# Kernel optimization log

Measured on AMD Instinct MI355X. Metric: run time of the kernel, lower is better.

Reference implementation:

```python
import jax, jax.numpy as jnp
import numpy as np

HEADS = 8
GROUPS = 8            # offset_groups (defaults to heads)
DIM = 256
DIM_HEAD = 64
INNER = HEADS * DIM_HEAD          # 512
OFF_DIMS = INNER // GROUPS        # 64
DS = 4                            # downsample_factor
OFF_SCALE = float(DS)             # offset_scale defaults to downsample_factor
KS = 6                            # offset_kernel_size
SCALE = DIM_HEAD ** -0.5


def grouped_conv1x1(x, w, groups):
    # x: (B, Cin, N), w: (Cout, Cin//groups, 1) -> (B, Cout, N)
    B, Cin, N = x.shape
    Cout = w.shape[0]
    xg = x.reshape(B, groups, Cin // groups, N)
    wg = w[:, :, 0].reshape(groups, Cout // groups, Cin // groups)
    return jnp.einsum('bgin,goi->bgon', xg, wg).reshape(B, Cout, N)


def group(t, groups):
    # 'b (g d) n -> (b g) d n'
    B, C, N = t.shape
    return t.reshape(B, groups, C // groups, N).reshape(B * groups, C // groups, N)


def bilinear_sample_1d(feats, grid):
    # F.grid_sample 1d equivalent: bilinear, padding_mode='zeros', align_corners=False
    # feats: (B, C, N); grid: (B, M) in [-1, 1] -> (B, C, M)
    B, C, N = feats.shape
    pos = ((grid + 1.0) * N - 1.0) * 0.5     # unnormalized coordinate
    i0f = jnp.floor(pos)
    w1 = (pos - i0f)[:, None, :]
    i0 = i0f.astype(jnp.int32)

    def gather(idx):
        valid = ((idx >= 0) & (idx < N))[:, None, :].astype(feats.dtype)
        g = jnp.take_along_axis(feats, jnp.clip(idx, 0, N - 1)[:, None, :], axis=2)
        return g * valid

    return gather(i0) * (1.0 - w1) + gather(i0 + 1) * w1


def setup_inputs() -> dict:
    key = jax.random.key(0)
    ks = jax.random.split(key, 10)
    B, N = 4, 4096
    s = lambda k, shape, fan: jax.random.normal(k, shape, jnp.float32) * (fan ** -0.5)
    return {
        'x': jax.random.normal(ks[0], (B, N, DIM), jnp.float32),
        'prev_x': jax.random.normal(ks[1], (B, N, DIM), jnp.float32),
        'wq': s(ks[2], (INNER, 2 * DIM // GROUPS, 1), 2 * DIM // GROUPS),
        'wk': s(ks[3], (INNER, DIM // GROUPS, 1), DIM // GROUPS),
        'wv': s(ks[4], (INNER, DIM // GROUPS, 1), DIM // GROUPS),
        'wo': s(ks[5], (DIM, INNER, 1), INNER),
        'bo': jnp.zeros((DIM,), jnp.float32),
        'w_off1': s(ks[6], (OFF_DIMS, 1, KS), KS),      # depthwise conv, groups=OFF_DIMS
        'b_off1': jnp.zeros((OFF_DIMS,), jnp.float32),
        'w_off2': s(ks[7], (1, OFF_DIMS, 1), OFF_DIMS),  # 1x1 conv, no bias
    }


def reference(x, prev_x, wq, wk, wv, wo, bo, w_off1, b_off1, w_off2):
    B, N, _ = x.shape
    xt = jnp.swapaxes(x, 1, 2)        # (B, D, N)
    pt = jnp.swapaxes(prev_x, 1, 2)   # (B, D, N)
    cat = jnp.concatenate([pt, xt], axis=1)       # (B, 2D, N)

    q = grouped_conv1x1(cat, wq, GROUPS)          # (B, INNER, N)
    gq = group(q, GROUPS)                         # (B*G, OFF_DIMS, N)

    # to_offsets: depthwise conv (stride DS) -> GELU -> 1x1 -> tanh -> *scale
    pad = (KS - DS) // 2
    h = jax.lax.conv_general_dilated(
        gq, w_off1, (DS,), [(pad, pad)],
        dimension_numbers=('NCH', 'OIH', 'NCH'),
        feature_group_count=OFF_DIMS)
    h = jax.nn.gelu(h + b_off1[None, :, None], approximate=False)  # (B*G, OFF_DIMS, M)
    offsets = jnp.einsum('bcn,oc->bon', h, w_off2[:, :, 0])[:, 0]  # (B*G, M)
    offsets = jnp.tanh(offsets) * OFF_SCALE

    M = offsets.shape[-1]                          # downsampled kv length
    vgrid = jnp.arange(M, dtype=offsets.dtype) + offsets
    vgrid_scaled = 2.0 * vgrid / max(M - 1, 1) - 1.0

    kv = bilinear_sample_1d(group(pt, GROUPS), vgrid_scaled)       # (B*G, D/G, M)
    kv = kv.reshape(B, GROUPS, DIM // GROUPS, M).reshape(B, DIM, M)

    k = grouped_conv1x1(kv, wk, GROUPS)            # (B, INNER, M)
    v = grouped_conv1x1(kv, wv, GROUPS)            # (B, INNER, M)

    # 'b (h d) n -> b h n d'
    qh = (q * SCALE).reshape(B, HEADS, DIM_HEAD, N).transpose(0, 1, 3, 2)
    kh = k.reshape(B, HEADS, DIM_HEAD, M).transpose(0, 1, 3, 2)
    vh = v.reshape(B, HEADS, DIM_HEAD, M).transpose(0, 1, 3, 2)

    attn = jax.nn.softmax(jnp.einsum('bhid,bhjd->bhij', qh, kh), axis=-1)
    out = jnp.einsum('bhij,bhjd->bhid', attn, vh)  # (B, H, N, Dh)

    out = out.transpose(0, 1, 3, 2).reshape(B, INNER, N)
    out = jnp.einsum('bcn,oc->bon', out, wo[:, :, 0]) + bo[None, :, None]
    return jnp.swapaxes(out, 1, 2)                 # (B, N, D)
```

## Files before the change

kernel.cpp:

```cpp
#include <hip/hip_runtime.h>
#include <hip/hip_bf16.h>

#define NN 4096
#define DIMC 256
#define NH 8
#define MM 1024
#define SCALE 0.18033688011112042f

typedef __hip_bfloat16 bf16;
typedef __bf16 bf16x8 __attribute__((ext_vector_type(8)));
typedef __bf16 bf16x4 __attribute__((ext_vector_type(4)));
typedef float f32x4 __attribute__((ext_vector_type(4)));
typedef unsigned u32x4 __attribute__((ext_vector_type(4)));
#define MFMA16(a, b, c) __builtin_amdgcn_mfma_f32_16x16x32_bf16(a, b, c, 0, 0, 0)

#define CVTPK(d, a, b) asm("v_cvt_pk_bf16_f32 %0, %1, %2" : "=v"(d) : "v"(a), "v"(b))
#define SWAP32(a, b) asm("v_permlane32_swap_b32 %0, %1" : "+v"(a), "+v"(b))
#define SWAP16(a, b) asm("v_permlane16_swap_b32 %0, %1" : "+v"(a), "+v"(b))

typedef __bf16 lds_row72[72];

__device__ __forceinline__ float bf2f(bf16 v) { return __bfloat162float(v); }
__device__ __forceinline__ float ldin(const void* p, size_t i, int f) {
    return f ? __bfloat162float(((const bf16*)p)[i]) : ((const float*)p)[i];
}
__device__ __forceinline__ bf16x8 ld8bf(const void* p, size_t i, int f) {
    if (f) return *(const bf16x8*)((const __bf16*)p + i);
    const float* s = (const float*)p + i;
    float4 a = *(const float4*)s, b = *(const float4*)(s + 4);
    bf16x8 r = {(__bf16)a.x, (__bf16)a.y, (__bf16)a.z, (__bf16)a.w,
                (__bf16)b.x, (__bf16)b.y, (__bf16)b.z, (__bf16)b.w};
    return r;
}

__global__ __launch_bounds__(256) void detect_kernel(const unsigned short* __restrict__ xu,
                                                     int* __restrict__ flag) {
    __shared__ int smax;
    int t = threadIdx.x;
    if (t == 0) smax = 0;
    __syncthreads();
    int mymax = 0;
    for (int i = t; i < 4096; i += 256) {
        int e = (xu[i] >> 7) & 0xFF;
        mymax = max(mymax, e);
    }
    atomicMax(&smax, mymax);
    __syncthreads();
    if (t == 0) *flag = (smax >= 0x90) ? 0 : 1;
}

__global__ __launch_bounds__(256) void off_kernel(
    const void* __restrict__ xp, const void* __restrict__ pxp,
    const void* __restrict__ wqp, const void* __restrict__ w1p,
    const void* __restrict__ b1p, const void* __restrict__ w2p,
    float* __restrict__ offs, const int* __restrict__ flagp) {
    __shared__ __align__(16) float wq_lds[64][68];
    __shared__ __align__(16) float cat_lds[66][68];
    __shared__ float q_lds[66][68];
    int f = *flagp;
    int t = threadIdx.x;
    int bg = blockIdx.x >> 6;
    int m0 = (blockIdx.x & 63) << 4;
    int b = bg >> 3, g = bg & 7;
    const void* src = (g < 4) ? pxp : xp;
    int base = (g & 3) << 6;
    for (int idx = t; idx < 4096; idx += 256)
        wq_lds[idx >> 6][idx & 63] = ldin(wqp, g * 4096 + idx, f);
    for (int idx = t; idx < 66 * 64; idx += 256) {
        int r = idx >> 6, c = idx & 63;
        int n = 4 * m0 - 1 + r;
        cat_lds[r][c] = (n >= 0 && n < NN)
            ? ldin(src, ((size_t)b * NN + n) * DIMC + base + c, f) : 0.0f;
    }
    __syncthreads();
    {
        int tc = t & 15, tr = t >> 4;
        float acc[4][4];
#pragma unroll
        for (int a = 0; a < 4; ++a)
#pragma unroll
            for (int bb = 0; bb < 4; ++bb) acc[a][bb] = 0.f;
#pragma unroll
        for (int i4 = 0; i4 < 16; ++i4) {
            float4 cv[4], wv[4];
#pragma unroll
            for (int a = 0; a < 4; ++a)
                cv[a] = *(const float4*)&cat_lds[tr + 16 * a][i4 * 4];
#pragma unroll
            for (int bb = 0; bb < 4; ++bb)
                wv[bb] = *(const float4*)&wq_lds[tc + 16 * bb][i4 * 4];
#pragma unroll
            for (int a = 0; a < 4; ++a)
#pragma unroll
                for (int bb = 0; bb < 4; ++bb) {
                    acc[a][bb] += cv[a].x * wv[bb].x;
                    acc[a][bb] += cv[a].y * wv[bb].y;
                    acc[a][bb] += cv[a].z * wv[bb].z;
                    acc[a][bb] += cv[a].w * wv[bb].w;
                }
        }
#pragma unroll
        for (int a = 0; a < 4; ++a)
#pragma unroll
            for (int bb = 0; bb < 4; ++bb)
                q_lds[tr + 16 * a][tc + 16 * bb] = acc[a][bb];
        if (t < 128) {
            int r = 64 + (t >> 6), c = t & 63;
            float a2 = 0.f;
#pragma unroll
            for (int i4 = 0; i4 < 16; ++i4) {
                float4 cv = *(const float4*)&cat_lds[r][i4 * 4];
                float4 wv = *(const float4*)&wq_lds[c][i4 * 4];
                a2 += cv.x * wv.x;
                a2 += cv.y * wv.y;
                a2 += cv.z * wv.z;
                a2 += cv.w * wv.w;
            }
            q_lds[r][c] = a2;
        }
    }
    __syncthreads();
    int w = t >> 6, lane = t & 63;
    float w1v[6];
#pragma unroll
    for (int tap = 0; tap < 6; ++tap) w1v[tap] = ldin(w1p, lane * 6 + tap, f);
    float b1v = ldin(b1p, lane, f);
    float w2v = ldin(w2p, lane, f);
    for (int jj = 0; jj < 4; ++jj) {
        int dm = w * 4 + jj;
        int r0 = 4 * dm;
        float acc = b1v;
#pragma unroll
        for (int tap = 0; tap < 6; ++tap) acc += q_lds[r0 + tap][lane] * w1v[tap];
        float gl = 0.5f * acc * (1.0f + erff(acc * 0.70710678118654752f));
        float s = gl * w2v;
#pragma unroll
        for (int o = 32; o; o >>= 1) s += __shfl_xor(s, o);
        if (lane == 0) offs[bg * MM + m0 + dm] = tanhf(s) * 4.0f;
    }
}

__global__ __launch_bounds__(256) void kvproj_kernel(
    const void* __restrict__ pxp, const void* __restrict__ wkp,
    const void* __restrict__ wvp, const float* __restrict__ offs,
    __bf16* __restrict__ khi_g, __bf16* __restrict__ klo_g,
    __bf16* __restrict__ vt_g, const int* __restrict__ flagp) {
    __shared__ float wk_lds[64][33];
    __shared__ float wv_lds[64][33];
    __shared__ float kv_lds[64][33];
    __shared__ __align__(16) __bf16 vt_lds[64][72];
    __shared__ float offl[64];
    int f = *flagp;
    int t = threadIdx.x;
    int bh = blockIdx.x >> 4;
    int m0 = (blockIdx.x & 15) << 6;
    int b = bh >> 3, h = bh & 7;
    if (t < 64) offl[t] = offs[bh * MM + m0 + t];
    for (int kk = t; kk < 2048; kk += 256) {
        wk_lds[kk >> 5][kk & 31] = ldin(wkp, h * 2048 + kk, f);
        wv_lds[kk >> 5][kk & 31] = ldin(wvp, h * 2048 + kk, f);
    }
    __syncthreads();
    for (int idx = t; idx < 2048; idx += 256) {
        int ml = idx >> 5, i = idx & 31;
        int m = m0 + ml;
        float off = offl[ml];
        float vgrid = (float)m + off;
        float gridn = 2.0f * vgrid / 1023.0f - 1.0f;
        float pos = ((gridn + 1.0f) * 4096.0f - 1.0f) * 0.5f;
        float i0f = floorf(pos);
        float w1 = pos - i0f;
        int i0 = (int)i0f;
        size_t basep = (size_t)b * NN * DIMC + h * 32 + i;
        float v0 = (i0 >= 0 && i0 < NN) ? ldin(pxp, basep + (size_t)i0 * DIMC, f) : 0.0f;
        int i1 = i0 + 1;
        float v1 = (i1 >= 0 && i1 < NN) ? ldin(pxp, basep + (size_t)i1 * DIMC, f) : 0.0f;
        kv_lds[ml][i] = v0 * (1.0f - w1) + v1 * w1;
    }
    __syncthreads();
    int d = t & 63, msub = t >> 6;
    for (int mc = 0; mc < 16; ++mc) {
        int ml = mc * 4 + msub;
        float ak = 0.f, av = 0.f;
#pragma unroll
        for (int i = 0; i < 32; ++i) {
            float x = kv_lds[ml][i];
            ak += x * wk_lds[d][i];
            av += x * wv_lds[d][i];
        }
        int m = m0 + ml;
        __bf16 kh = (__bf16)ak;
        khi_g[(size_t)(bh * MM + m) * 64 + d] = kh;
        klo_g[(size_t)(bh * MM + m) * 64 + d] = (__bf16)(ak - (float)kh);
        vt_lds[d][ml] = (__bf16)av;
    }
    __syncthreads();
    for (int idx = t; idx < 512; idx += 256) {
        int r = idx >> 3, c8 = (idx & 7) * 8;
        *(bf16x8*)&vt_g[((size_t)bh * 64 + r) * MM + m0 + c8] =
            *(const bf16x8*)&vt_lds[r][c8];
    }
}

__global__ __launch_bounds__(256, 4) void attn_kernel(
    const void* __restrict__ xp, const void* __restrict__ pxp,
    const void* __restrict__ wqp, const __bf16* __restrict__ khi_g,
    const __bf16* __restrict__ klo_g, const __bf16* __restrict__ vt_g,
    __bf16* __restrict__ ofb, const int* __restrict__ flagp) {
    __shared__ __align__(16) char smem[36864];
    int f = *flagp;
    int bh = blockIdx.x >> 5;
    int n0 = (blockIdx.x & 31) << 7;
    int b = bh >> 3, h = bh & 7;
    int t = threadIdx.x;
    int w = t >> 6, lane = t & 63;
    int quad = lane >> 4, l15 = lane & 15;

    lds_row72* x_lds  = (lds_row72*)smem;
    lds_row72* wq_lds = (lds_row72*)(smem + 18432);
    const void* src = (h < 4) ? pxp : xp;
    int cbase = (h & 3) << 6;
#pragma unroll
    for (int j = 0; j < 4; ++j) {
        int idx = t + j * 256;
        int r = idx >> 3, c8 = (idx & 7) * 8;
        *(bf16x8*)&x_lds[r][c8] =
            ld8bf(src, ((size_t)b * NN + n0 + r) * DIMC + cbase + c8, f);
    }
#pragma unroll
    for (int j = 0; j < 2; ++j) {
        int idx = t + j * 256;
        int r = idx >> 3, c8 = (idx & 7) * 8;
        *(bf16x8*)&wq_lds[r][c8] = ld8bf(wqp, h * 4096 + r * 64 + c8, f);
    }
    __syncthreads();
    bf16x8 axf[2][2], bwf[4][2];
#pragma unroll
    for (int ms = 0; ms < 2; ++ms)
#pragma unroll
        for (int ks = 0; ks < 2; ++ks)
            axf[ms][ks] = *(const bf16x8*)&x_lds[w * 32 + ms * 16 + l15][quad * 8 + ks * 32];
#pragma unroll
    for (int ns = 0; ns < 4; ++ns)
#pragma unroll
        for (int ks = 0; ks < 2; ++ks)
            bwf[ns][ks] = *(const bf16x8*)&wq_lds[ns * 16 + l15][quad * 8 + ks * 32];
    __syncthreads();
    lds_row72* qhi = (lds_row72*)smem;
    lds_row72* qlo = (lds_row72*)(smem + 18432);
#pragma unroll
    for (int ms = 0; ms < 2; ++ms)
#pragma unroll
        for (int ns = 0; ns < 4; ++ns) {
            f32x4 acc = {0.f, 0.f, 0.f, 0.f};
            acc = MFMA16(axf[ms][0], bwf[ns][0], acc);
            acc = MFMA16(axf[ms][1], bwf[ns][1], acc);
            int col = ns * 16 + l15;
#pragma unroll
            for (int reg = 0; reg < 4; ++reg) {
                int row = w * 32 + ms * 16 + quad * 4 + reg;
                float v = acc[reg] * SCALE;
                __bf16 hi = (__bf16)v;
                qhi[row][col] = hi;
                qlo[row][col] = (__bf16)(v - (float)hi);
            }
        }
    __syncthreads();
    bf16x8 qh[2][2], ql[2][2];
#pragma unroll
    for (int ms = 0; ms < 2; ++ms)
#pragma unroll
        for (int ks = 0; ks < 2; ++ks) {
            qh[ms][ks] = *(const bf16x8*)&qhi[w * 32 + ms * 16 + l15][quad * 8 + ks * 32];
            ql[ms][ks] = *(const bf16x8*)&qlo[w * 32 + ms * 16 + l15][quad * 8 + ks * 32];
        }

    lds_row72* khi = (lds_row72*)smem;
    lds_row72* klo = (lds_row72*)(smem + 9216);
    lds_row72* vt  = (lds_row72*)(smem + 18432);

    float l_run[2] = {0.f, 0.f};
    f32x4 oc[2][4];
#pragma unroll
    for (int ms = 0; ms < 2; ++ms)
#pragma unroll
        for (int nd = 0; nd < 4; ++nd) oc[ms][nd] = (f32x4){0.f, 0.f, 0.f, 0.f};

    const __bf16* khb = khi_g + (size_t)bh * MM * 64;
    const __bf16* klb = klo_g + (size_t)bh * MM * 64;
    const __bf16* vtb = vt_g + (size_t)bh * 64 * MM;

    int pr0 = t >> 3, pc0 = (t & 7) * 8;
    int pr1 = (t + 256) >> 3, pc1 = pc0;
    bf16x8 pk[2], pl[2], pv[2];
    {
        pk[0] = *(const bf16x8*)&khb[(size_t)pr0 * 64 + pc0];
        pk[1] = *(const bf16x8*)&khb[(size_t)pr1 * 64 + pc1];
        pl[0] = *(const bf16x8*)&klb[(size_t)pr0 * 64 + pc0];
        pl[1] = *(const bf16x8*)&klb[(size_t)pr1 * 64 + pc1];
        pv[0] = *(const bf16x8*)&vtb[(size_t)pr0 * MM + pc0];
        pv[1] = *(const bf16x8*)&vtb[(size_t)pr1 * MM + pc1];
    }

    for (int mt = 0; mt < 16; ++mt) {
        __syncthreads();
        *(bf16x8*)&khi[pr0][pc0] = pk[0];
        *(bf16x8*)&khi[pr1][pc1] = pk[1];
        *(bf16x8*)&klo[pr0][pc0] = pl[0];
        *(bf16x8*)&klo[pr1][pc1] = pl[1];
        *(bf16x8*)&vt[pr0][pc0]  = pv[0];
        *(bf16x8*)&vt[pr1][pc1]  = pv[1];
        __syncthreads();
        if (mt < 15) {
            int m1 = (mt + 1) * 64;
            pk[0] = *(const bf16x8*)&khb[(size_t)(m1 + pr0) * 64 + pc0];
            pk[1] = *(const bf16x8*)&khb[(size_t)(m1 + pr1) * 64 + pc1];
            pl[0] = *(const bf16x8*)&klb[(size_t)(m1 + pr0) * 64 + pc0];
            pl[1] = *(const bf16x8*)&klb[(size_t)(m1 + pr1) * 64 + pc1];
            pv[0] = *(const bf16x8*)&vtb[(size_t)pr0 * MM + m1 + pc0];
            pv[1] = *(const bf16x8*)&vtb[(size_t)pr1 * MM + m1 + pc1];
        }
        f32x4 s[2][4];
#pragma unroll
        for (int ms = 0; ms < 2; ++ms)
#pragma unroll
            for (int nk = 0; nk < 4; ++nk) s[ms][nk] = (f32x4){0.f, 0.f, 0.f, 0.f};
#pragma unroll
        for (int nk = 0; nk < 4; ++nk)
#pragma unroll
            for (int ks = 0; ks < 2; ++ks) {
                bf16x8 kh = *(const bf16x8*)&khi[nk * 16 + l15][quad * 8 + ks * 32];
                bf16x8 kl = *(const bf16x8*)&klo[nk * 16 + l15][quad * 8 + ks * 32];
#pragma unroll
                for (int ms = 0; ms < 2; ++ms) {
                    s[ms][nk] = MFMA16(kh, qh[ms][ks], s[ms][nk]);
                    s[ms][nk] = MFMA16(kl, qh[ms][ks], s[ms][nk]);
                    s[ms][nk] = MFMA16(kh, ql[ms][ks], s[ms][nk]);
                }
            }
        bf16x8 pf[2][2];
#pragma unroll
        for (int ms = 0; ms < 2; ++ms) {
            float ps = 0.f;
#pragma unroll
            for (int nk = 0; nk < 4; ++nk)
#pragma unroll
                for (int reg = 0; reg < 4; ++reg) {
                    float v = exp2f(s[ms][nk][reg] - 16.f);
                    s[ms][nk][reg] = v;
                    ps += v;
                }
            ps += __shfl_xor(ps, 16);
            ps += __shfl_xor(ps, 32);
            l_run[ms] += ps;
#pragma unroll
            for (int ks = 0; ks < 2; ++ks) {
                unsigned a0, a1, b0, b1;
                CVTPK(a0, s[ms][2 * ks][0], s[ms][2 * ks][1]);
                CVTPK(a1, s[ms][2 * ks][2], s[ms][2 * ks][3]);
                CVTPK(b0, s[ms][2 * ks + 1][0], s[ms][2 * ks + 1][1]);
                CVTPK(b1, s[ms][2 * ks + 1][2], s[ms][2 * ks + 1][3]);
                SWAP32(a0, b0);
                SWAP32(a1, b1);
                SWAP16(a0, b0);
                SWAP16(a1, b1);
                u32x4 wrd = {a0, a1, b0, b1};
                pf[ms][ks] = *(const bf16x8*)&wrd;
            }
        }
#pragma unroll
        for (int nd = 0; nd < 4; ++nd)
#pragma unroll
            for (int ks = 0; ks < 2; ++ks) {
                bf16x8 vf_ = *(const bf16x8*)&vt[nd * 16 + l15][quad * 8 + ks * 32];
#pragma unroll
                for (int ms = 0; ms < 2; ++ms)
                    oc[ms][nd] = MFMA16(pf[ms][ks], vf_, oc[ms][nd]);
            }
    }
#pragma unroll
    for (int ms = 0; ms < 2; ++ms)
#pragma unroll
        for (int reg = 0; reg < 4; ++reg) {
            float lsum = __shfl(l_run[ms], quad * 4 + reg);
            float rl = 1.0f / lsum;
            int n = n0 + w * 32 + ms * 16 + quad * 4 + reg;
#pragma unroll
            for (int nd = 0; nd < 4; ++nd)
                ofb[((size_t)b * NN + n) * 512 + h * 64 + nd * 16 + l15] =
                    (__bf16)(oc[ms][nd][reg] * rl);
        }
}

__global__ __launch_bounds__(256) void o_proj_kernel(
    const __bf16* __restrict__ ofb, const void* __restrict__ wop,
    const void* __restrict__ bop, void* __restrict__ out,
    const int* __restrict__ flagp) {
    __shared__ __align__(16) char smem[27648];
    lds_row72* ahi = (lds_row72*)smem;
    lds_row72* bwo = (lds_row72*)(smem + 18432);
    int f = *flagp;
    int t = threadIdx.x;
    int row0 = (blockIdx.x >> 2) * 128;
    int o0 = (blockIdx.x & 3) * 64;
    int w = t >> 6, lane = t & 63;
    int quad = lane >> 4, l15 = lane & 15;

    f32x4 oc[2][4];
#pragma unroll
    for (int ms = 0; ms < 2; ++ms)
#pragma unroll
        for (int nd = 0; nd < 4; ++nd) oc[ms][nd] = (f32x4){0.f, 0.f, 0.f, 0.f};

    for (int k0 = 0; k0 < 512; k0 += 64) {
        if (k0) __syncthreads();
#pragma unroll
        for (int j = 0; j < 4; ++j) {
            int idx = t + j * 256;
            int r = idx >> 3, c8 = (idx & 7) * 8;
            *(bf16x8*)&ahi[r][c8] =
                *(const bf16x8*)&ofb[(size_t)(row0 + r) * 512 + k0 + c8];
        }
#pragma unroll
        for (int j = 0; j < 2; ++j) {
            int idx = t + j * 256;
            int o = idx >> 3, c8 = (idx & 7) * 8;
            *(bf16x8*)&bwo[o][c8] = ld8bf(wop, (size_t)(o0 + o) * 512 + k0 + c8, f);
        }
        __syncthreads();
        bf16x8 af[2][2], bf_[4][2];
#pragma unroll
        for (int ms = 0; ms < 2; ++ms)
#pragma unroll
            for (int ks = 0; ks < 2; ++ks)
                af[ms][ks] = *(const bf16x8*)&ahi[w * 32 + ms * 16 + l15][quad * 8 + ks * 32];
#pragma unroll
        for (int nd = 0; nd < 4; ++nd)
#pragma unroll
            for (int ks = 0; ks < 2; ++ks)
                bf_[nd][ks] = *(const bf16x8*)&bwo[nd * 16 + l15][quad * 8 + ks * 32];
#pragma unroll
        for (int ms = 0; ms < 2; ++ms)
#pragma unroll
            for (int nd = 0; nd < 4; ++nd)
#pragma unroll
                for (int ks = 0; ks < 2; ++ks)
                    oc[ms][nd] = MFMA16(af[ms][ks], bf_[nd][ks], oc[ms][nd]);
    }
    float bias[4];
#pragma unroll
    for (int nd = 0; nd < 4; ++nd) bias[nd] = ldin(bop, o0 + nd * 16 + l15, f);
#pragma unroll
    for (int ms = 0; ms < 2; ++ms)
#pragma unroll
        for (int reg = 0; reg < 4; ++reg) {
            int grow = row0 + w * 32 + ms * 16 + quad * 4 + reg;
#pragma unroll
            for (int nd = 0; nd < 4; ++nd) {
                float v = oc[ms][nd][reg] + bias[nd];
                int o = o0 + nd * 16 + l15;
                if (f) ((bf16*)out)[(size_t)grow * 256 + o] = __float2bfloat16(v);
                else   ((float*)out)[(size_t)grow * 256 + o] = v;
            }
        }
}

extern "C" void kernel_launch(void* const* d_in, const int* in_sizes, int n_in,
                              void* d_out, int out_size, void* d_ws, size_t ws_size,
                              hipStream_t stream) {
    char* W = (char*)d_ws;
    int* flag = (int*)W;
    __bf16* khi_g = (__bf16*)(W + 256);
    __bf16* klo_g = khi_g + 2097152;
    __bf16* vt_g  = klo_g + 2097152;
    __bf16* ofb   = vt_g + 2097152;
    float* offs = (float*)(ofb + 8388608);

    hipLaunchKernelGGL(detect_kernel, dim3(1), dim3(256), 0, stream,
                       (const unsigned short*)d_in[0], flag);
    hipLaunchKernelGGL(off_kernel, dim3(2048), dim3(256), 0, stream,
                       d_in[0], d_in[1], d_in[2], d_in[7], d_in[8], d_in[9],
                       offs, flag);
    hipLaunchKernelGGL(kvproj_kernel, dim3(512), dim3(256), 0, stream,
                       d_in[1], d_in[3], d_in[4], offs, khi_g, klo_g, vt_g, flag);
    hipLaunchKernelGGL(attn_kernel, dim3(1024), dim3(256), 0, stream,
                       d_in[0], d_in[1], d_in[2], khi_g, klo_g, vt_g, ofb, flag);
    hipLaunchKernelGGL(o_proj_kernel, dim3(512), dim3(256), 0, stream,
                       ofb, d_in[5], d_in[6], d_out, flag);
}
```

Measured before the change: 265.7 us.

## Halve attention query tile and KV tile to raise occupancy; cache kv weights in registers

The attention kernel now handles 64 query rows per block instead of 128 and streams K/V in 32-row tiles instead of 64. This halves shared memory and register use and lets launch bounds request 8 blocks per CU, with twice as many blocks launched. The aim is to improve latency hiding for the attention stage. In exchange, each K/V tile is loaded from global memory by twice as many blocks and the loop runs twice as many iterations with barriers. Separately, the kv projection keeps its weight columns in registers instead of rereading them from LDS, and s_setprio hints are placed around the MFMA sections.

Result: slower. 387.2 us (+45.7%).

```diff
diff --git a/kernel.cpp b/kernel.cpp
--- a/kernel.cpp
+++ b/kernel.cpp
@@ -19,6 +19,7 @@
 #define SWAP16(a, b) asm("v_permlane16_swap_b32 %0, %1" : "+v"(a), "+v"(b))
 
 typedef __bf16 lds_row72[72];
+typedef __bf16 lds_row40[40];
 
 __device__ __forceinline__ float bf2f(bf16 v) { return __bfloat162float(v); }
 __device__ __forceinline__ float ldin(const void* p, size_t i, int f) {
@@ -179,14 +180,20 @@
     }
     __syncthreads();
     int d = t & 63, msub = t >> 6;
+    float wkr[32], wvr[32];
+#pragma unroll
+    for (int i = 0; i < 32; ++i) {
+        wkr[i] = wk_lds[d][i];
+        wvr[i] = wv_lds[d][i];
+    }
     for (int mc = 0; mc < 16; ++mc) {
         int ml = mc * 4 + msub;
         float ak = 0.f, av = 0.f;
 #pragma unroll
         for (int i = 0; i < 32; ++i) {
             float x = kv_lds[ml][i];
-            ak += x * wk_lds[d][i];
-            av += x * wv_lds[d][i];
+            ak += x * wkr[i];
+            av += x * wvr[i];
         }
         int m = m0 + ml;
         __bf16 kh = (__bf16)ak;
@@ -202,44 +209,37 @@
     }
 }
 
-__global__ __launch_bounds__(256, 4) void attn_kernel(
+__global__ __launch_bounds__(256, 8) void attn_kernel(
     const void* __restrict__ xp, const void* __restrict__ pxp,
     const void* __restrict__ wqp, const __bf16* __restrict__ khi_g,
     const __bf16* __restrict__ klo_g, const __bf16* __restrict__ vt_g,
     __bf16* __restrict__ ofb, const int* __restrict__ flagp) {
-    __shared__ __align__(16) char smem[36864];
+    __shared__ __align__(16) char smem[18432];
     int f = *flagp;
-    int bh = blockIdx.x >> 5;
-    int n0 = (blockIdx.x & 31) << 7;
+    int bh = blockIdx.x >> 6;
+    int n0 = (blockIdx.x & 63) << 6;
     int b = bh >> 3, h = bh & 7;
     int t = threadIdx.x;
     int w = t >> 6, lane = t & 63;
     int quad = lane >> 4, l15 = lane & 15;
 
     lds_row72* x_lds  = (lds_row72*)smem;
-    lds_row72* wq_lds = (lds_row72*)(smem + 18432);
+    lds_row72* wq_lds = (lds_row72*)(smem + 9216);
     const void* src = (h < 4) ? pxp : xp;
     int cbase = (h & 3) << 6;
 #pragma unroll
-    for (int j = 0; j < 4; ++j) {
+    for (int j = 0; j < 2; ++j) {
         int idx = t + j * 256;
         int r = idx >> 3, c8 = (idx & 7) * 8;
         *(bf16x8*)&x_lds[r][c8] =
             ld8bf(src, ((size_t)b * NN + n0 + r) * DIMC + cbase + c8, f);
-    }
-#pragma unroll
-    for (int j = 0; j < 2; ++j) {
-        int idx = t + j * 256;
-        int r = idx >> 3, c8 = (idx & 7) * 8;
         *(bf16x8*)&wq_lds[r][c8] = ld8bf(wqp, h * 4096 + r * 64 + c8, f);
     }
     __syncthreads();
-    bf16x8 axf[2][2], bwf[4][2];
-#pragma unroll
-    for (int ms = 0; ms < 2; ++ms)
-#pragma unroll
-        for (int ks = 0; ks < 2; ++ks)
-            axf[ms][ks] = *(const bf16x8*)&x_lds[w * 32 + ms * 16 + l15][quad * 8 + ks * 32];
+    bf16x8 axf[2], bwf[4][2];
+#pragma unroll
+    for (int ks = 0; ks < 2; ++ks)
+        axf[ks] = *(const bf16x8*)&x_lds[w * 16 + l15][quad * 8 + ks * 32];
 #pragma unroll
     for (int ns = 0; ns < 4; ++ns)
 #pragma unroll
@@ -247,149 +247,118 @@
             bwf[ns][ks] = *(const bf16x8*)&wq_lds[ns * 16 + l15][quad * 8 + ks * 32];
     __syncthreads();
     lds_row72* qhi = (lds_row72*)smem;
-    lds_row72* qlo = (lds_row72*)(smem + 18432);
-#pragma unroll
-    for (int ms = 0; ms < 2; ++ms)
-#pragma unroll
-        for (int ns = 0; ns < 4; ++ns) {
-            f32x4 acc = {0.f, 0.f, 0.f, 0.f};
-            acc = MFMA16(axf[ms][0], bwf[ns][0], acc);
-            acc = MFMA16(axf[ms][1], bwf[ns][1], acc);
-            int col = ns * 16 + l15;
-#pragma unroll
-            for (int reg = 0; reg < 4; ++reg) {
-                int row = w * 32 + ms * 16 + quad * 4 + reg;
-                float v = acc[reg] * SCALE;
-                __bf16 hi = (__bf16)v;
-                qhi[row][col] = hi;
-                qlo[row][col] = (__bf16)(v - (float)hi);
-            }
-        }
-    __syncthreads();
-    bf16x8 qh[2][2], ql[2][2];
-#pragma unroll
-    for (int ms = 0; ms < 2; ++ms)
-#pragma unroll
-        for (int ks = 0; ks < 2; ++ks) {
-            qh[ms][ks] = *(const bf16x8*)&qhi[w * 32 + ms * 16 + l15][quad * 8 + ks * 32];
-            ql[ms][ks] = *(const bf16x8*)&qlo[w * 32 + ms * 16 + l15][quad * 8 + ks * 32];
-        }
+    lds_row72* qlo = (lds_row72*)(smem + 9216);
+#pragma unroll
+    for (int ns = 0; ns < 4; ++ns) {
+        f32x4 acc = {0.f, 0.f, 0.f, 0.f};
+        acc = MFMA16(axf[0], bwf[ns][0], acc);
+        acc = MFMA16(axf[1], bwf[ns][1], acc);
+        int col = ns * 16 + l15;
+#pragma unroll
+        for (int reg = 0; reg < 4; ++reg) {
+            int row = w * 16 + quad * 4 + reg;
+            float v = acc[reg] * SCALE;
+            __bf16 hi = (__bf16)v;
+            qhi[row][col] = hi;
+            qlo[row][col] = (__bf16)(v - (float)hi);
+        }
+    }
+    __syncthreads();
+    bf16x8 qh[2], ql[2];
+#pragma unroll
+    for (int ks = 0; ks < 2; ++ks) {
+        qh[ks] = *(const bf16x8*)&qhi[w * 16 + l15][quad * 8 + ks * 32];
+        ql[ks] = *(const bf16x8*)&qlo[w * 16 + l15][quad * 8 + ks * 32];
+    }
 
     lds_row72* khi = (lds_row72*)smem;
-    lds_row72* klo = (lds_row72*)(smem + 9216);
-    lds_row72* vt  = (lds_row72*)(smem + 18432);
-
-    float l_run[2] = {0.f, 0.f};
-    f32x4 oc[2][4];
-#pragma unroll
-    for (int ms = 0; ms < 2; ++ms)
-#pragma unroll
-        for (int nd = 0; nd < 4; ++nd) oc[ms][nd] = (f32x4){0.f, 0.f, 0.f, 0.f};
+    lds_row72* klo = (lds_row72*)(smem + 4608);
+    lds_row40* vt  = (lds_row40*)(smem + 9216);
+
+    float l_run = 0.f;
+    f32x4 oc[4];
+#pragma unroll
+    for (int nd = 0; nd < 4; ++nd) oc[nd] = (f32x4){0.f, 0.f, 0.f, 0.f};
 
     const __bf16* khb = khi_g + (size_t)bh * MM * 64;
     const __bf16* klb = klo_g + (size_t)bh * MM * 64;
     const __bf16* vtb = vt_g + (size_t)bh * 64 * MM;
 
-    int pr0 = t >> 3, pc0 = (t & 7) * 8;
-    int pr1 = (t + 256) >> 3, pc1 = pc0;
-    bf16x8 pk[2], pl[2], pv[2];
-    {
-        pk[0] = *(const bf16x8*)&khb[(size_t)pr0 * 64 + pc0];
-        pk[1] = *(const bf16x8*)&khb[(size_t)pr1 * 64 + pc1];
-        pl[0] = *(const bf16x8*)&klb[(size_t)pr0 * 64 + pc0];
-        pl[1] = *(const bf16x8*)&klb[(size_t)pr1 * 64 + pc1];
-        pv[0] = *(const bf16x8*)&vtb[(size_t)pr0 * MM + pc0];
-        pv[1] = *(const bf16x8*)&vtb[(size_t)pr1 * MM + pc1];
-    }
-
-    for (int mt = 0; mt < 16; ++mt) {
+    int kr = t >> 3, kc = (t & 7) * 8;
+    int vr = t >> 2, vc = (t & 3) * 8;
+    bf16x8 pk, pl, pv;
+    pk = *(const bf16x8*)&khb[(size_t)kr * 64 + kc];
+    pl = *(const bf16x8*)&klb[(size_t)kr * 64 + kc];
+    pv = *(const bf16x8*)&vtb[(size_t)vr * MM + vc];
+
+    for (int mt = 0; mt < 32; ++mt) {
         __syncthreads();
-        *(bf16x8*)&khi[pr0][pc0] = pk[0];
-        *(bf16x8*)&khi[pr1][pc1] = pk[1];
-        *(bf16x8*)&klo[pr0][pc0] = pl[0];
-        *(bf16x8*)&klo[pr1][pc1] = pl[1];
-        *(bf16x8*)&vt[pr0][pc0]  = pv[0];
-        *(bf16x8*)&vt[pr1][pc1]  = pv[1];
+        *(bf16x8*)&khi[kr][kc] = pk;
+        *(bf16x8*)&klo[kr][kc] = pl;
+        *(bf16x8*)&vt[vr][vc]  = pv;
         __syncthreads();
-        if (mt < 15) {
-            int m1 = (mt + 1) * 64;
-            pk[0] = *(const bf16x8*)&khb[(size_t)(m1 + pr0) * 64 + pc0];
-            pk[1] = *(const bf16x8*)&khb[(size_t)(m1 + pr1) * 64 + pc1];
-            pl[0] = *(const bf16x8*)&klb[(size_t)(m1 + pr0) * 64 + pc0];
-            pl[1] = *(const bf16x8*)&klb[(size_t)(m1 + pr1) * 64 + pc1];
-            pv[0] = *(const bf16x8*)&vtb[(size_t)pr0 * MM + m1 + pc0];
-            pv[1] = *(const bf16x8*)&vtb[(size_t)pr1 * MM + m1 + pc1];
-        }
-        f32x4 s[2][4];
-#pragma unroll
-        for (int ms = 0; ms < 2; ++ms)
-#pragma unroll
-            for (int nk = 0; nk < 4; ++nk) s[ms][nk] = (f32x4){0.f, 0.f, 0.f, 0.f};
-#pragma unroll
-        for (int nk = 0; nk < 4; ++nk)
+        if (mt < 31) {
+            int m1 = (mt + 1) * 32;
+            pk = *(const bf16x8*)&khb[(size_t)(m1 + kr) * 64 + kc];
+            pl = *(const bf16x8*)&klb[(size_t)(m1 + kr) * 64 + kc];
+            pv = *(const bf16x8*)&vtb[(size_t)vr * MM + m1 + vc];
+        }
+        f32x4 s[2];
+        s[0] = (f32x4){0.f, 0.f, 0.f, 0.f};
+        s[1] = (f32x4){0.f, 0.f, 0.f, 0.f};
+        __builtin_amdgcn_s_setprio(1);
+#pragma unroll
+        for (int nk = 0; nk < 2; ++nk)
 #pragma unroll
             for (int ks = 0; ks < 2; ++ks) {
                 bf16x8 kh = *(const bf16x8*)&khi[nk * 16 + l15][quad * 8 + ks * 32];
                 bf16x8 kl = *(const bf16x8*)&klo[nk * 16 + l15][quad * 8 + ks * 32];
-#pragma unroll
-                for (int ms = 0; ms < 2; ++ms) {
-                    s[ms][nk] = MFMA16(kh, qh[ms][ks], s[ms][nk]);
-                    s[ms][nk] = MFMA16(kl, qh[ms][ks], s[ms][nk]);
-                    s[ms][nk] = MFMA16(kh, ql[ms][ks], s[ms][nk]);
-                }
+                s[nk] = MFMA16(kh, qh[ks], s[nk]);
+                s[nk] = MFMA16(kl, qh[ks], s[nk]);
+                s[nk] = MFMA16(kh, ql[ks], s[nk]);
             }
-        bf16x8 pf[2][2];
-#pragma unroll
-        for (int ms = 0; ms < 2; ++ms) {
-            float ps = 0.f;
-#pragma unroll
-            for (int nk = 0; nk < 4; ++nk)
-#pragma unroll
-                for (int reg = 0; reg < 4; ++reg) {
-                    float v = exp2f(s[ms][nk][reg] - 16.f);
-                    s[ms][nk][reg] = v;
-                    ps += v;
-                }
-            ps += __shfl_xor(ps, 16);
-            ps += __shfl_xor(ps, 32);
-            l_run[ms] += ps;
-#pragma unroll
-            for (int ks = 0; ks < 2; ++ks) {
-                unsigned a0, a1, b0, b1;
-                CVTPK(a0, s[ms][2 * ks][0], s[ms][2 * ks][1]);
-                CVTPK(a1, s[ms][2 * ks][2], s[ms][2 * ks][3]);
-                CVTPK(b0, s[ms][2 * ks + 1][0], s[ms][2 * ks + 1][1]);
-                CVTPK(b1, s[ms][2 * ks + 1][2], s[ms][2 * ks + 1][3]);
-                SWAP32(a0, b0);
-                SWAP32(a1, b1);
-                SWAP16(a0, b0);
-                SWAP16(a1, b1);
-                u32x4 wrd = {a0, a1, b0, b1};
-                pf[ms][ks] = *(const bf16x8*)&wrd;
+        __builtin_amdgcn_s_setprio(0);
+        float ps = 0.f;
+#pragma unroll
+        for (int nk = 0; nk < 2; ++nk)
+#pragma unroll
+            for (int reg = 0; reg < 4; ++reg) {
+                float v = exp2f(s[nk][reg] - 16.f);
+                s[nk][reg] = v;
+                ps += v;
             }
-        }
+        ps += __shfl_xor(ps, 16);
+        ps += __shfl_xor(ps, 32);
+        l_run += ps;
+        unsigned a0, a1, b0, b1;
+        CVTPK(a0, s[0][0], s[0][1]);
+        CVTPK(a1, s[0][2], s[0][3]);
+        CVTPK(b0, s[1][0], s[1][1]);
+        CVTPK(b1, s[1][2], s[1][3]);
+        SWAP32(a0, b0);
+        SWAP32(a1, b1);
+        SWAP16(a0, b0);
+        SWAP16(a1, b1);
+        u32x4 wrd = {a0, a1, b0, b1};
+        bf16x8 pf = *(const bf16x8*)&wrd;
+        __builtin_amdgcn_s_setprio(1);
+#pragma unroll
+        for (int nd = 0; nd < 4; ++nd) {
+            bf16x8 vf_ = *(const bf16x8*)&vt[nd * 16 + l15][quad * 8];
+            oc[nd] = MFMA16(pf, vf_, oc[nd]);
+        }
+        __builtin_amdgcn_s_setprio(0);
+    }
+#pragma unroll
+    for (int reg = 0; reg < 4; ++reg) {
+        float lsum = __shfl(l_run, quad * 4 + reg);
+        float rl = 1.0f / lsum;
+        int n = n0 + w * 16 + quad * 4 + reg;
 #pragma unroll
         for (int nd = 0; nd < 4; ++nd)
-#pragma unroll
-            for (int ks = 0; ks < 2; ++ks) {
-                bf16x8 vf_ = *(const bf16x8*)&vt[nd * 16 + l15][quad * 8 + ks * 32];
-#pragma unroll
-                for (int ms = 0; ms < 2; ++ms)
-                    oc[ms][nd] = MFMA16(pf[ms][ks], vf_, oc[ms][nd]);
-            }
-    }
-#pragma unroll
-    for (int ms = 0; ms < 2; ++ms)
-#pragma unroll
-        for (int reg = 0; reg < 4; ++reg) {
-            float lsum = __shfl(l_run[ms], quad * 4 + reg);
-            float rl = 1.0f / lsum;
-            int n = n0 + w * 32 + ms * 16 + quad * 4 + reg;
-#pragma unroll
-            for (int nd = 0; nd < 4; ++nd)
-                ofb[((size_t)b * NN + n) * 512 + h * 64 + nd * 16 + l15] =
-                    (__bf16)(oc[ms][nd][reg] * rl);
-        }
+            ofb[((size_t)b * NN + n) * 512 + h * 64 + nd * 16 + l15] =
+                (__bf16)(oc[nd][reg] * rl);
+    }
 }
 
 __global__ __launch_bounds__(256) void o_proj_kernel(
@@ -483,7 +452,7 @@
                        offs, flag);
     hipLaunchKernelGGL(kvproj_kernel, dim3(512), dim3(256), 0, stream,
                        d_in[1], d_in[3], d_in[4], offs, khi_g, klo_g, vt_g, flag);
-    hipLaunchKernelGGL(attn_kernel, dim3(1024), dim3(256), 0, stream,
+    hipLaunchKernelGGL(attn_kernel, dim3(2048), dim3(256), 0, stream,
                        d_in[0], d_in[1], d_in[2], khi_g, klo_g, vt_g, ofb, flag);
     hipLaunchKernelGGL(o_proj_kernel, dim3(512), dim3(256), 0, stream,
                        ofb, d_in[5], d_in[6], d_out, flag);
```
